# Kernel optimization log

Measured on AMD Instinct MI355X. Metric: run time of the kernel, lower is better.

Reference implementation:

```python
import jax, jax.numpy as jnp
import numpy as np

BATCH, T, S, M = 512, 4096, 64, 125  # batch, seq_len, n_states, emission alphabet (5^3)


def setup_inputs() -> dict:
    key = jax.random.key(0)
    k1, k2, k3, k4 = jax.random.split(key, 4)
    obs = jax.random.randint(k1, (BATCH, T), 0, M)
    x = jax.nn.one_hot(obs, M, dtype=jnp.float32)            # [B, T, M] one-hot emissions
    I = jax.nn.softmax(jax.random.normal(k2, (1, S)))        # initial state distribution [1, S]
    A = jax.nn.softmax(jax.random.normal(k3, (S, S)), axis=-1)   # transition matrix, rows sum to 1
    Bm = jax.nn.softmax(jax.random.normal(k4, (M, S)), axis=0)   # emission matrix, cols sum to 1
    return {"x": x, "I": I, "A": A, "Bm": Bm}


def reference(x, I, A, Bm):
    """HMM forward algorithm with per-step normalization (default scaling branch of CgpHmmCell).

    Returns the accumulated log-likelihood [B, 1].
    """
    xT = jnp.swapaxes(x, 0, 1)  # [T, B, M] for scan over time

    # t = 1: R = I (broadcast over batch), old_loglik = 0
    E0 = xT[0] @ Bm                                  # [B, S]
    u0 = E0 * I                                      # unscaled alpha
    Z0 = jnp.sum(u0, axis=1, keepdims=True)          # [B, 1]
    carry0 = (u0 / Z0, jnp.log(Z0))

    def step(carry, x_t):
        alpha, ll = carry
        R = alpha @ A                                # [B, S] transition
        E = x_t @ Bm                                 # [B, S] emission lookup (one-hot matmul)
        u = E * R
        Z = jnp.sum(u, axis=1, keepdims=True)        # per-sequence scaling factor
        return (u / Z, ll + jnp.log(Z)), None

    (alpha, loglik), _ = jax.lax.scan(step, carry0, xT[1:])
    return loglik
```

## Files before the change

kernel.cpp:

```cpp
#include <hip/hip_runtime.h>


#define BATCH 512
#define T 4096
#define S 64
#define M 125
#define NPACK 10
#define BURNP 2
#define WPB 4
#define RB 56.0f
#define SCALEF 7.205759403792794e16f

typedef __attribute__((ext_vector_type(8))) short bf16x8;
typedef __attribute__((ext_vector_type(4))) float f32x4;

union BFU { unsigned u[4]; bf16x8 v; };

__device__ __forceinline__ unsigned pk_trunc(float a, float b) {
    return (__float_as_uint(b) & 0xFFFF0000u) | (__float_as_uint(a) >> 16);
}
__device__ __forceinline__ unsigned pk_rne(float a, float b) {
    unsigned ua = __float_as_uint(a); ua += 0x7FFFu + ((ua >> 16) & 1u);
    unsigned ub = __float_as_uint(b); ub += 0x7FFFu + ((ub >> 16) & 1u);
    return (ub & 0xFFFF0000u) | (ua >> 16);
}

__global__ __launch_bounds__(256) void hmm_fused(const float* __restrict__ x,
                                                 const float* __restrict__ Iv,
                                                 const float* __restrict__ A,
                                                 const float* __restrict__ Bm,
                                                 float* __restrict__ out) {
    __shared__ __align__(16) float BmL[M * S];
    __shared__ __align__(16) float ILds[S];
    __shared__ unsigned long long ulds[WPB * 16 * NPACK];

    const int tid = threadIdx.x, wv = tid >> 6, lane = tid & 63;
    const int s = lane & 15, g = lane >> 4;

    for (int i = tid; i < M * S; i += WPB * 64) BmL[i] = Bm[i];
    if (tid < S) ILds[tid] = Iv[tid];
    __syncthreads();

    BFU Af[4][2];
#pragma unroll
    for (int mt = 0; mt < 4; ++mt)
#pragma unroll
        for (int kf = 0; kf < 2; ++kf)
#pragma unroll
            for (int j2 = 0; j2 < 4; ++j2) {
                int p0 = 32 * kf + 16 * (j2 >> 1) + 4 * g + 2 * (j2 & 1);
                Af[mt][kf].u[j2] = pk_rne(A[(size_t)p0 * S + mt * 16 + s],
                                          A[(size_t)(p0 + 1) * S + mt * 16 + s]);
            }

    const int W = blockIdx.x * WPB + wv;
    const int seq = W >> 2, wq = W & 3;
    const float* xs = x + (size_t)seq * T * M;
    unsigned long long* myu = &ulds[wv * 16 * NPACK];
    const int base = wq * 1024;

    float bufA[16], bufB[16];

    auto issue16 = [&](int r0a, int r0b) {
#pragma unroll
        for (int j = 0; j < 8; ++j) {
            unsigned ra = (unsigned)((r0a + j) * 125);
            unsigned rb = (unsigned)((r0b + j) * 125);
            bufA[j] = xs[ra + lane];       bufB[j] = xs[ra + 61 + lane];
            bufA[8 + j] = xs[rb + lane];   bufB[8 + j] = xs[rb + 61 + lane];
        }
    };
    auto ext8 = [&](int jb) -> unsigned long long {
        unsigned long long acc = 0;
#pragma unroll
        for (int j = 0; j < 8; ++j) {
            unsigned long long mA = __ballot(bufA[jb + j] != 0.0f);
            unsigned long long mB = __ballot(bufB[jb + j] != 0.0f);
            int o = mA ? (int)__builtin_ctzll(mA) : 61 + (int)__builtin_ctzll(mB);
            acc |= (unsigned long long)o << (8 * j);
        }
        return acc;
    };
    auto put = [&](int st, int pt, unsigned long long v) {
        if (lane == st) myu[st * NPACK + pt] = v;
    };

    {
        int pa = base - 16, pb = base - 8;
        if (pa < 0) pa = 0;
        if (pb < 0) pb = 0;
        issue16(pa, pb);
        for (int gi = 0; gi <= 16; ++gi) {
            unsigned long long a0 = ext8(0), a1 = ext8(8);
            if (gi < 16) {
                int ni = gi + 1;
                if (ni <= 8) { int i = ni - 1; issue16(base + (2 * i) * 64 + 48, base + (2 * i + 1) * 64 + 48); }
                else         { int i = ni - 9; issue16(base + (2 * i) * 64 + 56, base + (2 * i + 1) * 64 + 56); }
            } else {
                issue16(base + 0, base + 64);
            }
            if (gi == 0) {
                put(0, 0, a0); put(0, 1, a1);
            } else if (gi <= 8) {
                int i = gi - 1;
                put(2 * i, 8, a0);     put(2 * i + 1, 0, a0);
                put(2 * i + 1, 8, a1); if (2 * i + 2 <= 15) put(2 * i + 2, 0, a1);
            } else {
                int i = gi - 9;
                put(2 * i, 9, a0);     put(2 * i + 1, 1, a0);
                put(2 * i + 1, 9, a1); if (2 * i + 2 <= 15) put(2 * i + 2, 1, a1);
            }
        }
    }

    BFU Bf[2];
#pragma unroll
    for (int kf = 0; kf < 2; ++kf)
#pragma unroll
        for (int j = 0; j < 4; ++j) Bf[kf].u[j] = 0x3F803F80u;

    float S0v = 0.f, swv = 1.f;

    for (int p = 0; p < NPACK; ++p) {
        unsigned long long uv = myu[s * NPACK + p];
        const bool exsl = (p < 6);
        for (int k = 0; k < 8; ++k) {
            if (exsl) {
                unsigned long long a0 = ext8(0), a1 = ext8(8);
                int np = (k == 7) ? p + 1 : p, nk = (k + 1) & 7;
                if (np < 6)
                    issue16(base + (2 * nk) * 64 + 8 * np,
                            base + (2 * nk + 1) * 64 + 8 * np);
                put(2 * k, p + 2, a0);
                put(2 * k + 1, p + 2, a1);
            }
            const int o = (int)(uv & 255ull);
            uv >>= 8;
            const float* br = &BmL[o << 6];
            f32x4 E[4];
#pragma unroll
            for (int mt = 0; mt < 4; ++mt)
                E[mt] = *(const f32x4*)&br[mt * 16 + g * 4];
            float w[4][4];
#pragma unroll
            for (int mt = 0; mt < 4; ++mt) {
                f32x4 zr = {0.f, 0.f, 0.f, 0.f};
                f32x4 z0 = __builtin_amdgcn_mfma_f32_16x16x32_bf16(Af[mt][0].v, Bf[0].v, zr, 0, 0, 0);
                f32x4 z1 = __builtin_amdgcn_mfma_f32_16x16x32_bf16(Af[mt][1].v, Bf[1].v, zr, 0, 0, 0);
#pragma unroll
                for (int r = 0; r < 4; ++r) w[mt][r] = (z0[r] + z1[r]) * E[mt][r];
            }
            if (p == BURNP && k == 0 && wq == 0) {
                const bool c0 = (s == 0);
#pragma unroll
                for (int mt = 0; mt < 4; ++mt)
#pragma unroll
                    for (int r = 0; r < 4; ++r)
                        w[mt][r] = c0 ? ILds[mt * 16 + g * 4 + r] * E[mt][r] : w[mt][r];
            }
            if (k == 7 && (p == BURNP - 1 || p == NPACK - 1)) {
                float swl = 0.f;
#pragma unroll
                for (int mt = 0; mt < 4; ++mt)
#pragma unroll
                    for (int r = 0; r < 4; ++r) swl += w[mt][r];
                swl += __shfl_xor(swl, 16);
                swl += __shfl_xor(swl, 32);
                swv = swl;
            }
#pragma unroll
            for (int kf = 0; kf < 2; ++kf)
#pragma unroll
                for (int j2 = 0; j2 < 4; ++j2) {
                    int mt = 2 * kf + (j2 >> 1), pr = j2 & 1;
                    float v0 = w[mt][2 * pr], v1 = w[mt][2 * pr + 1];
                    if (k == 7) { v0 *= SCALEF; v1 *= SCALEF; }
                    Bf[kf].u[j2] = pk_trunc(v0, v1);
                }
        }
        if (p == BURNP - 1) {
            const bool ch0 = (wq == 0) && (s == 0);
            S0v = ch0 ? ((float)(NPACK - 1 - BURNP) * RB)
                      : (__log2f(swv) + (float)(NPACK - BURNP) * RB);
        }
    }

    float tot = __log2f(swv) - S0v;
    tot += __shfl_xor(tot, 1);
    tot += __shfl_xor(tot, 2);
    tot += __shfl_xor(tot, 4);
    tot += __shfl_xor(tot, 8);
    if (lane == 0)
        atomicAdd(out + seq, tot * 0.6931471805599453f);
}

extern "C" void kernel_launch(void* const* d_in, const int* in_sizes, int n_in,
                              void* d_out, int out_size, void* d_ws, size_t ws_size,
                              hipStream_t stream) {
    const float* x  = (const float*)d_in[0];
    const float* I  = (const float*)d_in[1];
    const float* A  = (const float*)d_in[2];
    const float* Bm = (const float*)d_in[3];
    float* out = (float*)d_out;
    (void)d_ws; (void)ws_size;

    hipMemsetAsync(out, 0, (size_t)out_size * sizeof(float), stream);
    hmm_fused<<<(BATCH * 4) / WPB, WPB * 64, 0, stream>>>(x, I, A, Bm, out);
}
```

Before: 1.309 ms.

## Vectorize one-hot row loads and overlap MFMA issue with index extraction

The one-hot extraction now loads each 125-float emission row as unaligned float4 vectors, with half a wavefront per row, so two rows fit in one ballot. The emitted index is recovered with a per-lane candidate and readlane, which cuts the ballot and load count. The MFMA transition products and the emission-row LDS reads are now issued before the index-extraction work in each step, so the matrix latency can overlap it. The cost is unaligned vector loads, with the last lane's load overlapping the previous lane's, plus extra readlane operations.

```diff
diff --git a/kernel.cpp b/kernel.cpp
--- a/kernel.cpp
+++ b/kernel.cpp
@@ -13,6 +13,7 @@
 
 typedef __attribute__((ext_vector_type(8))) short bf16x8;
 typedef __attribute__((ext_vector_type(4))) float f32x4;
+typedef float f32x4u __attribute__((ext_vector_type(4), aligned(4)));
 
 union BFU { unsigned u[4]; bf16x8 v; };
 
@@ -59,25 +60,35 @@
     unsigned long long* myu = &ulds[wv * 16 * NPACK];
     const int base = wq * 1024;
 
-    float bufA[16], bufB[16];
+    const int rel = lane & 31, hf = lane >> 5;
+    const unsigned coff = (rel < 31) ? 4u * (unsigned)rel : 121u;
+
+    f32x4u buf4[8];
 
     auto issue16 = [&](int r0a, int r0b) {
 #pragma unroll
-        for (int j = 0; j < 8; ++j) {
-            unsigned ra = (unsigned)((r0a + j) * 125);
-            unsigned rb = (unsigned)((r0b + j) * 125);
-            bufA[j] = xs[ra + lane];       bufB[j] = xs[ra + 61 + lane];
-            bufA[8 + j] = xs[rb + lane];   bufB[8 + j] = xs[rb + 61 + lane];
+        for (int j = 0; j < 4; ++j) {
+            unsigned ra = (unsigned)((r0a + 2 * j + hf) * 125) + coff;
+            unsigned rb = (unsigned)((r0b + 2 * j + hf) * 125) + coff;
+            buf4[j]     = *(const f32x4u*)&xs[ra];
+            buf4[4 + j] = *(const f32x4u*)&xs[rb];
         }
     };
-    auto ext8 = [&](int jb) -> unsigned long long {
+    auto ext8 = [&](int b) -> unsigned long long {
         unsigned long long acc = 0;
 #pragma unroll
-        for (int j = 0; j < 8; ++j) {
-            unsigned long long mA = __ballot(bufA[jb + j] != 0.0f);
-            unsigned long long mB = __ballot(bufB[jb + j] != 0.0f);
-            int o = mA ? (int)__builtin_ctzll(mA) : 61 + (int)__builtin_ctzll(mB);
-            acc |= (unsigned long long)o << (8 * j);
+        for (int j = 0; j < 4; ++j) {
+            f32x4u v = buf4[b * 4 + j];
+            bool nz = (v.x != 0.f) || (v.y != 0.f) || (v.z != 0.f) || (v.w != 0.f);
+            unsigned li = (v.x != 0.f) ? 0u : ((v.y != 0.f) ? 1u : ((v.z != 0.f) ? 2u : 3u));
+            unsigned cand = coff + li;
+            unsigned long long m = __ballot(nz);
+            unsigned l0 = (unsigned)__builtin_ctzll(m & 0xffffffffull);
+            unsigned l1 = (unsigned)__builtin_ctzll(m >> 32);
+            unsigned o0 = __builtin_amdgcn_readlane(cand, l0);
+            unsigned o1 = __builtin_amdgcn_readlane(cand, 32 + l1);
+            acc |= ((unsigned long long)o0 << (16 * j)) |
+                   ((unsigned long long)o1 << (16 * j + 8));
         }
         return acc;
     };
@@ -91,7 +102,7 @@
         if (pb < 0) pb = 0;
         issue16(pa, pb);
         for (int gi = 0; gi <= 16; ++gi) {
-            unsigned long long a0 = ext8(0), a1 = ext8(8);
+            unsigned long long a0 = ext8(0), a1 = ext8(1);
             if (gi < 16) {
                 int ni = gi + 1;
                 if (ni <= 8) { int i = ni - 1; issue16(base + (2 * i) * 64 + 48, base + (2 * i + 1) * 64 + 48); }
@@ -125,8 +136,19 @@
         unsigned long long uv = myu[s * NPACK + p];
         const bool exsl = (p < 6);
         for (int k = 0; k < 8; ++k) {
+            const int o = (int)(uv & 255ull);
+            uv >>= 8;
+            const float* br = &BmL[o << 6];
+            f32x4 E[4], z0[4], z1[4];
+#pragma unroll
+            for (int mt = 0; mt < 4; ++mt) {
+                E[mt] = *(const f32x4*)&br[mt * 16 + g * 4];
+                f32x4 zr = {0.f, 0.f, 0.f, 0.f};
+                z0[mt] = __builtin_amdgcn_mfma_f32_16x16x32_bf16(Af[mt][0].v, Bf[0].v, zr, 0, 0, 0);
+                z1[mt] = __builtin_amdgcn_mfma_f32_16x16x32_bf16(Af[mt][1].v, Bf[1].v, zr, 0, 0, 0);
+            }
             if (exsl) {
-                unsigned long long a0 = ext8(0), a1 = ext8(8);
+                unsigned long long a0 = ext8(0), a1 = ext8(1);
                 int np = (k == 7) ? p + 1 : p, nk = (k + 1) & 7;
                 if (np < 6)
                     issue16(base + (2 * nk) * 64 + 8 * np,
@@ -134,22 +156,11 @@
                 put(2 * k, p + 2, a0);
                 put(2 * k + 1, p + 2, a1);
             }
-            const int o = (int)(uv & 255ull);
-            uv >>= 8;
-            const float* br = &BmL[o << 6];
-            f32x4 E[4];
+            float w[4][4];
 #pragma unroll
             for (int mt = 0; mt < 4; ++mt)
-                E[mt] = *(const f32x4*)&br[mt * 16 + g * 4];
-            float w[4][4];
-#pragma unroll
-            for (int mt = 0; mt < 4; ++mt) {
-                f32x4 zr = {0.f, 0.f, 0.f, 0.f};
-                f32x4 z0 = __builtin_amdgcn_mfma_f32_16x16x32_bf16(Af[mt][0].v, Bf[0].v, zr, 0, 0, 0);
-                f32x4 z1 = __builtin_amdgcn_mfma_f32_16x16x32_bf16(Af[mt][1].v, Bf[1].v, zr, 0, 0, 0);
-#pragma unroll
-                for (int r = 0; r < 4; ++r) w[mt][r] = (z0[r] + z1[r]) * E[mt][r];
-            }
+#pragma unroll
+                for (int r = 0; r < 4; ++r) w[mt][r] = (z0[mt][r] + z1[mt][r]) * E[mt][r];
             if (p == BURNP && k == 0 && wq == 0) {
                 const bool c0 = (s == 0);
 #pragma unroll
```

New measurement: 1.305 ms. Within noise of the previous version (-0.3%).
